# Kernel tuning notes

Measured on AMD Instinct MI355X. Metric: run time of the kernel, lower is better.

The kernel has to match this reference:

```python
import jax, jax.numpy as jnp
import numpy as np

N, E = 20000, 640000
D_IN, D_H, D_OUT = 128, 64, 32


def _lin_w(key, out_d, in_d):
    return jax.random.normal(key, (out_d, in_d), jnp.float32) / np.sqrt(in_d)


def setup_inputs() -> dict:
    key = jax.random.key(0)
    ks = jax.random.split(key, 16)
    x = jax.random.normal(ks[0], (N, D_IN), jnp.float32)
    edge_index = jax.random.randint(ks[1], (2, E), 0, N, jnp.int64)
    inp = {"x": x, "edge_index": edge_index}
    # SAGEConv weights: lin_l (aggregated neighbors, with bias), lin_r (root, no bias)
    inp["Wl1"] = _lin_w(ks[2], D_H, D_IN); inp["bl1"] = jnp.zeros((D_H,), jnp.float32)
    inp["Wr1"] = _lin_w(ks[3], D_H, D_IN)
    inp["Wl2"] = _lin_w(ks[4], D_H, D_H); inp["bl2"] = jnp.zeros((D_H,), jnp.float32)
    inp["Wr2"] = _lin_w(ks[5], D_H, D_H)
    inp["Wl3"] = _lin_w(ks[6], D_OUT, D_H); inp["bl3"] = jnp.zeros((D_OUT,), jnp.float32)
    inp["Wr3"] = _lin_w(ks[7], D_OUT, D_H)
    # Conv2d kernels (OIHW), all 3x3 pad 1
    inp["Wc1"] = jax.random.normal(ks[8], (D_H, 1, 3, 3), jnp.float32) / 3.0
    inp["bc1"] = jnp.zeros((D_H,), jnp.float32)
    inp["Wc2"] = jax.random.normal(ks[9], (D_H, D_H, 3, 3), jnp.float32) / np.sqrt(9 * D_H)
    inp["bc2"] = jnp.zeros((D_H,), jnp.float32)
    inp["Wc3"] = jax.random.normal(ks[10], (1, D_H, 3, 3), jnp.float32) / np.sqrt(9 * D_H)
    inp["bc3"] = jnp.zeros((1,), jnp.float32)
    # linear2 (hidden -> hidden)
    inp["W2"] = _lin_w(ks[11], D_H, D_H); inp["b2"] = jnp.zeros((D_H,), jnp.float32)
    return inp


def _sage(x, src, dst, Wl, bl, Wr):
    # PyG SAGEConv (mean aggr): lin_l(mean_{j->i} x_j) + lin_r(x_i)
    msg = x[src]  # [E, d] gather
    agg = jax.ops.segment_sum(msg, dst, num_segments=N)
    deg = jax.ops.segment_sum(jnp.ones((src.shape[0], 1), x.dtype), dst, num_segments=N)
    agg = agg / jnp.maximum(deg, 1.0)
    return agg @ Wl.T + bl + x @ Wr.T


def _conv(x, w, b):
    y = jax.lax.conv_general_dilated(x, w, (1, 1), ((1, 1), (1, 1)),
                                     dimension_numbers=("NCHW", "OIHW", "NCHW"))
    return y + b[None, :, None, None]


def reference(x, edge_index, Wl1, bl1, Wr1, Wl2, bl2, Wr2, Wl3, bl3, Wr3,
              Wc1, bc1, Wc2, bc2, Wc3, bc3, W2, b2):
    src, dst = edge_index[0], edge_index[1]
    h = _sage(x, src, dst, Wl1, bl1, Wr1)
    h = _sage(h, src, dst, Wl2, bl2, Wr2)
    h = _sage(h, src, dst, Wl2, bl2, Wr2)  # sage2 reused, as in source
    out_1 = h
    h4 = h[None, None]                     # [1,1,N,D_H]
    out = _conv(h4, Wc1, bc1)              # [1,D_H,N,D_H]
    out = _conv(out, Wc2, bc2)             # dropout is identity at inference
    out = _conv(out, Wc3, bc3)             # [1,1,N,D_H]
    out = out[0, 0] + out_1
    out = out @ W2.T + b2
    h = _sage(out, src, dst, Wl2, bl2, Wr2)
    h = _sage(h, src, dst, Wl2, bl2, Wr2)
    h = _sage(h, src, dst, Wl3, bl3, Wr3)
    return h
```

## Files before the change

kernel.cpp:

```cpp
#include <hip/hip_runtime.h>

#define NN 20000
#define NE 640000
#define NBUK 79

__device__ __forceinline__ int probe_stride(const int* __restrict__ ei32) {
  int lane = threadIdx.x & 63;
  int v = ei32[2 * lane + 1];
  unsigned long long nz = __ballot(v != 0);
  return (nz == 0ull) ? 2 : 1;
}

__device__ __forceinline__ bool maskB(int var, int o2, int o1) {
  int s = o2 + o1;
  switch (var) {
    case 0: return (o2 >= 0) && (s >= 0);
    case 1: return s >= -1;
    case 3: return s <= 1;
    case 4: return (o2 <= 0) && (s <= 0);
    default: return true;
  }
}

__global__ __launch_bounds__(256) void k_phaseA1(
    const int* __restrict__ ei, int* __restrict__ bhist,
    const float* __restrict__ Wc1, const float* __restrict__ Wc2,
    const float* __restrict__ Wc3, const float* __restrict__ bc1,
    const float* __restrict__ bc2, const float* __restrict__ bc3,
    const float* __restrict__ Wl1, const float* __restrict__ Wr1,
    const float* __restrict__ Wl2, const float* __restrict__ Wr2,
    const float* __restrict__ bl2,
    float* __restrict__ T729, float* __restrict__ beta5,
    float* __restrict__ Wt1, float* __restrict__ Wt2,
    float* __restrict__ Sbuf, float* __restrict__ c5,
    int* __restrict__ rowptr, int E, int N) {
  __shared__ float smem[6336];
  int b = blockIdx.x, tid = threadIdx.x;
  if (b >= 151) {
    int* lb = (int*)smem;
    int st = probe_stride(ei);
    for (int i = tid; i < NBUK; i += 256) lb[i] = 0;
    __syncthreads();
    int u = b - 151;
    int e0 = u * 4096;
#pragma unroll
    for (int t = 0; t < 16; ++t) {
      int e = e0 + t * 256 + tid;
      if (e < E) atomicAdd(&lb[ei[(size_t)(E + e) * st] >> 8], 1);
    }
    __syncthreads();
    for (int i = tid; i < NBUK; i += 256) bhist[u * NBUK + i] = lb[i];
    return;
  }
  int s = b;
  if (s == 0) {
    float* W3  = smem;
    float* S9s = smem + 576;
    float* W1s = smem + 5760;
    if (tid == 0) rowptr[N] = E;
    for (int e = tid; e < 576; e += 256) { W3[e] = Wc3[e]; W1s[e] = Wc1[e]; }
    __syncthreads();
    for (int bb = tid; bb < 576; bb += 256) {
      float acc[9];
#pragma unroll
      for (int a = 0; a < 9; ++a) acc[a] = 0.0f;
#pragma unroll 4
      for (int o = 0; o < 64; ++o) {
        float w2 = Wc2[o * 576 + bb];
#pragma unroll
        for (int a = 0; a < 9; ++a) acc[a] += W3[o * 9 + a] * w2;
      }
#pragma unroll
      for (int a = 0; a < 9; ++a) S9s[a * 576 + bb] = acc[a];
    }
    __syncthreads();
    for (int c = tid; c < 729; c += 256) {
      int kx0  = c % 3;
      int dl1e = (c / 3) % 3;
      int dl2e = (c / 9) % 3;
      int ky0  = (c / 27) % 3;
      int ky1  = (c / 81) % 3;
      int ky2  = c / 243;
      const float* s9 = &S9s[(ky2 * 3 + dl2e) * 576 + ky1 * 3 + dl1e];
      const float* w1 = &W1s[ky0 * 3 + kx0];
      float t = 0.0f;
#pragma unroll 8
      for (int i = 0; i < 64; ++i) t += s9[i * 9] * w1[i * 9];
      T729[c] = t;
    }
  } else if (s <= 5) {
    float* S2   = smem;
    float* W3b  = smem + 576;
    float* B2   = smem + 1152;
    float* part = smem + 1216;
    int var = s - 1;
    for (int e = tid; e < 576; e += 256) {
      int o = e / 9, r = e - o * 9;
      float t = 0.0f;
      for (int i = 0; i < 64; ++i) t += Wc2[o * 576 + i * 9 + r] * bc1[i];
      S2[e] = t;
      W3b[e] = Wc3[e];
    }
    if (tid < 64) B2[tid] = bc2[tid];
    __syncthreads();
    int u = tid & 63, oc = tid >> 6;
    float acc = 0.0f;
    for (int ky2 = 0; ky2 < 3; ++ky2) {
      int o2 = ky2 - 1;
      bool okA = (var == 0) ? (o2 >= 0) : (var == 4) ? (o2 <= 0) : true;
      if (!okA) continue;
      for (int dl2 = -1; dl2 <= 1; ++dl2) {
        int p = u + dl2; if ((unsigned)p >= 64u) continue;
        float sel[9];
#pragma unroll
        for (int ky1 = 0; ky1 < 3; ++ky1) {
          int o1 = ky1 - 1;
          bool mb = maskB(var, o2, o1);
#pragma unroll
          for (int dl1 = -1; dl1 <= 1; ++dl1) {
            int pq = p + dl1;
            sel[ky1 * 3 + dl1 + 1] = (mb && (unsigned)pq < 64u) ? 1.0f : 0.0f;
          }
        }
#pragma unroll 4
        for (int oo = 0; oo < 16; ++oo) {
          int o = oc * 16 + oo;
          float inner = B2[o];
#pragma unroll
          for (int r = 0; r < 9; ++r) inner += S2[o * 9 + r] * sel[r];
          acc += W3b[o * 9 + ky2 * 3 + (dl2 + 1)] * inner;
        }
      }
    }
    part[tid] = acc;
    __syncthreads();
    if (tid < 64) {
      beta5[var * 64 + tid] =
          bc3[0] + part[tid] + part[64 + tid] + part[128 + tid] + part[192 + tid];
    }
  } else {
    int idx = (s - 6) * 256 + tid;
    if (idx < 16384) {
      int w = idx >> 7, u = idx & 127;
      Wt1[idx] = (u < 64) ? Wl1[u * 128 + w] : Wr1[(u - 64) * 128 + w];
    } else if (idx < 24576) {
      int t = idx - 16384;
      int w = t >> 7, u = t & 127;
      Wt2[t] = (u < 64) ? Wl2[u * 64 + w] : Wr2[(u - 64) * 64 + w];
    } else if (idx < 36864) {
      int t2 = idx - 24576;
      int m = t2 >> 12, e = t2 & 4095;
      int i = e >> 6, j = e & 63;
      float acc = 0.0f;
#pragma unroll 4
      for (int k = 0; k < 64; ++k) {
        float wlj = Wl2[j * 64 + k], wrj = Wr2[j * 64 + k];
        float wli = Wl2[k * 64 + i], wri = Wr2[k * 64 + i];
        if (m == 0) acc += wli * wlj;
        else if (m == 1) acc += wri * wlj + wli * wrj;
        else acc += wri * wrj;
      }
      Sbuf[t2] = acc;
    } else if (idx < 36928) {
      int j = idx - 36864;
      float acc = bl2[j];
      for (int i = 0; i < 64; ++i)
        acc += bl2[i] * (Wl2[j * 64 + i] + Wr2[j * 64 + i]);
      c5[j] = acc;
    }
  }
}

__global__ __launch_bounds__(256) void k_phaseA2(
    const float* __restrict__ X, const float* __restrict__ Wt1,
    float* __restrict__ yzA,
    const int* __restrict__ ei, const int* __restrict__ bhist,
    unsigned long long* __restrict__ ebuf,
    const float* __restrict__ T729, float* __restrict__ M5T,
    const float* __restrict__ Sbuf, const float* __restrict__ c5,
    const float* __restrict__ Wl3, const float* __restrict__ Wr3,
    const float* __restrict__ bl3, float* __restrict__ Gbuf,
    float* __restrict__ c32, int E, int N) {
  __shared__ float smem[2048];
  int b = blockIdx.x, tid = threadIdx.x;
  if (b < 157) {
    int* lcnt  = (int*)smem;
    int* lbase = (int*)smem + 128;
    int* sscan = (int*)smem + 256;
    int st = probe_stride(ei);
    for (int i = tid; i < NBUK; i += 256) lcnt[i] = 0;
    int tot = 0, myoff = 0;
    if (tid < NBUK) {
      for (int v = 0; v < 157; ++v) {
        int h = bhist[v * NBUK + tid];
        tot += h;
        if (v < b) myoff += h;
      }
    }
    if (tid < 128) sscan[tid] = (tid < NBUK) ? tot : 0;
    __syncthreads();
    for (int off = 1; off < 128; off <<= 1) {
      int v = 0;
      if (tid < 128 && tid >= off) v = sscan[tid - off];
      __syncthreads();
      if (tid < 128) sscan[tid] += v;
      __syncthreads();
    }
    if (tid < NBUK) lbase[tid] = (sscan[tid] - tot) + myoff;
    __syncthreads();
    int e0 = b * 4096;
    int srcv[16], dstv[16], lrank[16], bk[16];
    int n = 0;
#pragma unroll
    for (int t = 0; t < 16; ++t) {
      int e = e0 + t * 256 + tid;
      if (e < E) {
        int sv = ei[(size_t)e * st];
        int d = ei[(size_t)(E + e) * st];
        int bb = d >> 8;
        srcv[n] = sv; dstv[n] = d; bk[n] = bb;
        lrank[n] = atomicAdd(&lcnt[bb], 1);
        ++n;
      }
    }
    for (int t = 0; t < n; ++t) {
      int pos = lbase[bk[t]] + lrank[t];
      ebuf[pos] = ((unsigned long long)(unsigned)dstv[t] << 32) | (unsigned)srcv[t];
    }
  } else if (b < 219) {
    float* Ts = smem;
    for (int e = tid; e < 729; e += 256) Ts[e] = T729[e];
    __syncthreads();
    int idx = (b - 157) * 256 + tid;
    if (idx >= 15680) return;
    int jw = idx % 7;
    int u  = (idx / 7) % 64;
    int d  = (idx / 448) % 7;
    int var = idx / 3136;
    int w = u + jw - 3;
    float acc = 0.0f;
    if (w >= 0 && w < 64) {
      for (int ky2 = 0; ky2 < 3; ++ky2) {
        int o2 = ky2 - 1;
        for (int ky1 = 0; ky1 < 3; ++ky1) {
          int o1 = ky1 - 1;
          if (!maskB(var, o2, o1)) continue;
          int o0 = (d - 3) - o2 - o1;
          if (o0 < -1 || o0 > 1) continue;
          int ky0 = o0 + 1;
          int cbase = ((ky2 * 3 + ky1) * 3 + ky0) * 27;
#pragma unroll
          for (int kx0 = 0; kx0 < 3; ++kx0) {
            int jq = jw - kx0;
            if ((unsigned)jq >= 5u) continue;
            int q = u + jq - 2;
            if ((unsigned)q >= 64u) continue;
#pragma unroll
            for (int dl2e = 0; dl2e < 3; ++dl2e) {
              int p = u + dl2e - 1;
              if ((unsigned)p >= 64u) continue;
              int dl1e = jq - dl2e;
              if ((unsigned)dl1e >= 3u) continue;
              acc += Ts[cbase + dl2e * 9 + dl1e * 3 + kx0];
            }
          }
        }
      }
    }
    if (d == 3 && jw == 3) acc += 1.0f;
    M5T[(var * 49 + d * 7 + jw) * 64 + u] = acc;
  } else if (b < 252) {
    int bb = b - 219;
    if (bb < 32) {
      int idx = bb * 256 + tid;
      int kblk = idx >> 11;
      int rem = idx & 2047;
      int t = rem >> 5, j = rem & 31;
      const float* S2p = Sbuf;
      const float* S1p = Sbuf + 4096;
      const float* S0p = Sbuf + 8192;
      const float* pa = (kblk == 0) ? S2p : (kblk == 1) ? S1p : (kblk == 2) ? S0p : nullptr;
      const float* pb = (kblk == 1) ? S2p : (kblk == 2) ? S1p : (kblk == 3) ? S0p : nullptr;
      float acc = 0.0f;
#pragma unroll 4
      for (int k = 0; k < 64; ++k) {
        if (pa) acc += pa[t * 64 + k] * Wl3[j * 64 + k];
        if (pb) acc += pb[t * 64 + k] * Wr3[j * 64 + k];
      }
      Gbuf[idx] = acc;
    } else if (tid < 32) {
      float acc = bl3[tid];
      for (int k = 0; k < 64; ++k)
        acc += c5[k] * (Wl3[tid * 64 + k] + Wr3[tid * 64 + k]);
      c32[tid] = acc;
    }
  } else {
    constexpr int C = 128, K = 128, ROWS = 16, RPT = ROWS * C / 256;
    float* Xs = smem;
    int y0 = (b - 252) * ROWS;
    {
      const float4* src = (const float4*)(X + (size_t)y0 * K);
      float4* dst = (float4*)Xs;
#pragma unroll
      for (int v = 0; v < ROWS * K / 4 / 256; ++v)
        dst[v * 256 + tid] = src[v * 256 + tid];
    }
    __syncthreads();
    int u = tid % C;
    int rg = tid / C;
    float acc[RPT];
#pragma unroll
    for (int k = 0; k < RPT; ++k) acc[k] = 0.0f;
#pragma unroll 2
    for (int w0 = 0; w0 < K; w0 += 4) {
      float m0 = Wt1[(w0 + 0) * C + u];
      float m1 = Wt1[(w0 + 1) * C + u];
      float m2 = Wt1[(w0 + 2) * C + u];
      float m3 = Wt1[(w0 + 3) * C + u];
      const float* xs = &Xs[(rg * RPT) * K + w0];
#pragma unroll
      for (int k = 0; k < RPT; ++k) {
        float4 h = *(const float4*)(xs + k * K);
        acc[k] += m0 * h.x + m1 * h.y + m2 * h.z + m3 * h.w;
      }
    }
#pragma unroll
    for (int k = 0; k < RPT; ++k)
      yzA[(size_t)(y0 + rg * RPT + k) * C + u] = acc[k];
  }
}

__global__ __launch_bounds__(256) void k_phaseA3(
    const unsigned long long* __restrict__ ebuf, const int* __restrict__ bhist,
    int* __restrict__ rowptr, float* __restrict__ invdeg,
    int* __restrict__ csr,
    const float* __restrict__ Gbuf, const float* __restrict__ W2,
    const float* __restrict__ b2, float* __restrict__ Wg,
    float* __restrict__ bg, int N) {
  __shared__ int smem[772];
  int b = blockIdx.x, tid = threadIdx.x;
  if (b < NBUK) {
    int* lcnt  = smem;
    int* lcur  = smem + 256;
    int* wsum  = smem + 512;
    int* sscan = smem + 516;
    int* tots  = smem + 644;
    int tot = 0;
    if (tid < NBUK)
      for (int v = 0; v < 157; ++v) tot += bhist[v * NBUK + tid];
    if (tid < 128) { tots[tid] = (tid < NBUK) ? tot : 0; sscan[tid] = tots ? ((tid < NBUK) ? tot : 0) : 0; }
    __syncthreads();
    for (int off = 1; off < 128; off <<= 1) {
      int v = 0;
      if (tid < 128 && tid >= off) v = sscan[tid - off];
      __syncthreads();
      if (tid < 128) sscan[tid] += v;
      __syncthreads();
    }
    if (tid < 128) sscan[tid] -= tots[tid];
    __syncthreads();
    int base = sscan[b];
    int n = tots[b];
    lcnt[tid] = 0;
    __syncthreads();
    for (int e = tid; e < n; e += 256) {
      int d = (int)(ebuf[base + e] >> 32);
      atomicAdd(&lcnt[d - (b << 8)], 1);
    }
    __syncthreads();
    int c = lcnt[tid];
    int lane = tid & 63, wid = tid >> 6;
    int s = c;
#pragma unroll
    for (int off = 1; off < 64; off <<= 1) {
      int v = __shfl_up(s, off, 64);
      if (lane >= off) s += v;
    }
    if (lane == 63) wsum[wid] = s;
    __syncthreads();
    int woff = 0;
    for (int w = 0; w < wid; ++w) woff += wsum[w];
    int pref = woff + s - c;
    int gnode = (b << 8) + tid;
    if (gnode < N) {
      rowptr[gnode] = base + pref;
      invdeg[gnode] = 1.0f / (float)(c < 1 ? 1 : c);
    }
    lcur[tid] = pref;
    __syncthreads();
    for (int e = tid; e < n; e += 256) {
      unsigned long long pk = ebuf[base + e];
      int d = (int)(pk >> 32);
      int pos = atomicAdd(&lcur[d - (b << 8)], 1);
      csr[base + pos] = (int)(unsigned)pk;
    }
  } else {
    int bb = b - NBUK;
    if (bb < 32) {
      int idx = bb * 256 + tid;
      int w = idx >> 7, u = idx & 127;
      int kblk = u >> 5, j = u & 31;
      const float* gp = Gbuf + kblk * 2048 + j;
      float acc = 0.0f;
#pragma unroll 4
      for (int t = 0; t < 64; ++t) acc += W2[t * 64 + w] * gp[t * 32];
      Wg[idx] = acc;
    } else if (tid < 128) {
      int kblk = tid >> 5, j = tid & 31;
      const float* gp = Gbuf + kblk * 2048 + j;
      float acc = 0.0f;
      for (int t = 0; t < 64; ++t) acc += b2[t] * gp[t * 32];
      bg[tid] = acc;
    }
  }
}

template <int C>
__global__ __launch_bounds__(256) void k_fused(const float* __restrict__ yzin,
                                               const int* __restrict__ csr,
                                               const int* __restrict__ rowptr,
                                               const float* __restrict__ invdeg,
                                               const float* __restrict__ bl,
                                               const float* __restrict__ Wt,
                                               float* __restrict__ out, int N) {
  constexpr int FV = 16;
  constexpr int G  = 4;
  constexpr int S4 = 32;
  constexpr int CAP = 64;
  __shared__ int idxs[16 * CAP];
  __shared__ float htile[16 * 64];
  int tid = threadIdx.x;
  int w = tid >> 6, lane = tid & 63;
  int base = blockIdx.x * 16;
  int beg_r[4], m_r[4], end_r[4];
#pragma unroll
  for (int rr = 0; rr < 4; ++rr) {
    int node = base + w * 4 + rr;
    int beg = rowptr[node], end = rowptr[node + 1];
    beg_r[rr] = beg; end_r[rr] = end;
    int cnt = end - beg;
    int m = cnt < CAP ? cnt : CAP;
    m_r[rr] = m;
    int* my = &idxs[(w * 4 + rr) * CAP];
    for (int k = lane; k < m; k += 64) my[k] = csr[beg + k];
  }
  __syncthreads();
  int g = lane / FV, f = lane % FV;
  const float4* yz4 = (const float4*)yzin;
#pragma unroll
  for (int rr = 0; rr < 4; ++rr) {
    int node = base + w * 4 + rr;
    const int* my = &idxs[(w * 4 + rr) * CAP];
    int m = m_r[rr];
    float a0x=0,a0y=0,a0z=0,a0w=0, a1x=0,a1y=0,a1z=0,a1w=0;
    float a2x=0,a2y=0,a2z=0,a2w=0, a3x=0,a3y=0,a3z=0,a3w=0;
    int j = g;
    for (; j + 3 * G < m; j += 4 * G) {
      int s0 = my[j], s1 = my[j + G], s2 = my[j + 2 * G], s3 = my[j + 3 * G];
      float4 v0 = yz4[(size_t)s0 * S4 + f];
      float4 v1 = yz4[(size_t)s1 * S4 + f];
      float4 v2 = yz4[(size_t)s2 * S4 + f];
      float4 v3 = yz4[(size_t)s3 * S4 + f];
      a0x += v0.x; a0y += v0.y; a0z += v0.z; a0w += v0.w;
      a1x += v1.x; a1y += v1.y; a1z += v1.z; a1w += v1.w;
      a2x += v2.x; a2y += v2.y; a2z += v2.z; a2w += v2.w;
      a3x += v3.x; a3y += v3.y; a3z += v3.z; a3w += v3.w;
    }
    for (; j < m; j += G) {
      int s0 = my[j];
      float4 v0 = yz4[(size_t)s0 * S4 + f];
      a0x += v0.x; a0y += v0.y; a0z += v0.z; a0w += v0.w;
    }
    for (int jj = beg_r[rr] + CAP + g; jj < end_r[rr]; jj += G) {
      int s0 = csr[jj];
      float4 v0 = yz4[(size_t)s0 * S4 + f];
      a0x += v0.x; a0y += v0.y; a0z += v0.z; a0w += v0.w;
    }
    float ax = (a0x + a1x) + (a2x + a3x);
    float ay = (a0y + a1y) + (a2y + a3y);
    float az = (a0z + a1z) + (a2z + a3z);
    float aw = (a0w + a1w) + (a2w + a3w);
#pragma unroll
    for (int mm = FV; mm < 64; mm <<= 1) {
      ax += __shfl_xor(ax, mm, 64);
      ay += __shfl_xor(ay, mm, 64);
      az += __shfl_xor(az, mm, 64);
      aw += __shfl_xor(aw, mm, 64);
    }
    if (g == 0) {
      float4 root = yz4[(size_t)node * S4 + FV + f];
      float4 bv = ((const float4*)bl)[f];
      float id = invdeg[node];
      float4 o;
      o.x = ax * id + bv.x + root.x;
      o.y = ay * id + bv.y + root.y;
      o.z = az * id + bv.z + root.z;
      o.w = aw * id + bv.w + root.w;
      ((float4*)htile)[(w * 4 + rr) * 16 + f] = o;
    }
  }
  __syncthreads();
  constexpr int RPT = 16 * C / 256;
  int u = tid % C, rg = tid / C;
  float acc[RPT];
#pragma unroll
  for (int k = 0; k < RPT; ++k) acc[k] = 0.0f;
#pragma unroll 2
  for (int w0 = 0; w0 < 64; w0 += 4) {
    float m0 = Wt[(w0 + 0) * C + u];
    float m1 = Wt[(w0 + 1) * C + u];
    float m2 = Wt[(w0 + 2) * C + u];
    float m3 = Wt[(w0 + 3) * C + u];
    const float* xs = &htile[(rg * RPT) * 64 + w0];
#pragma unroll
    for (int k = 0; k < RPT; ++k) {
      float4 h4 = *(const float4*)(xs + k * 64);
      acc[k] += m0 * h4.x + m1 * h4.y + m2 * h4.z + m3 * h4.w;
    }
  }
#pragma unroll
  for (int k = 0; k < RPT; ++k)
    out[(size_t)(base + rg * RPT + k) * C + u] = acc[k];
}

__global__ __launch_bounds__(256) void k_applyfused(
    const float* __restrict__ h, const float* __restrict__ M5T,
    const float* __restrict__ beta5, const float* __restrict__ Wg,
    const float* __restrict__ bg, float* __restrict__ wout, int N) {
  __shared__ float hs[22 * 70];
  __shared__ float htile[16 * 64];
  int tid = threadIdx.x;
  int bstart = blockIdx.x * 16;
  for (int idx = tid; idx < 22 * 70; idx += 256) {
    int row = idx / 70, col = idx - row * 70;
    int y = bstart - 3 + row;
    int ww = col - 3;
    float v = 0.0f;
    if ((unsigned)y < (unsigned)N && (unsigned)ww < 64u)
      v = h[(size_t)y * 64 + ww];
    hs[idx] = v;
  }
  __syncthreads();
  int u = tid & 63, g = tid >> 6;
  int lr0 = g * 4;
  int gstart = bstart + lr0;
  const float* basep = &hs[lr0 * 70 + u];
  bool interior = (gstart >= 2) && (gstart + 3 <= N - 3);
  if (interior) {
    float c[49];
#pragma unroll
    for (int t = 0; t < 49; ++t) c[t] = M5T[(2 * 49 + t) * 64 + u];
    float bet = beta5[2 * 64 + u];
    float acc[4];
#pragma unroll
    for (int k = 0; k < 4; ++k) acc[k] = bet;
#pragma unroll
    for (int rr = 0; rr < 10; ++rr) {
      float t7[7];
#pragma unroll
      for (int jw = 0; jw < 7; ++jw) t7[jw] = basep[rr * 70 + jw];
#pragma unroll
      for (int d = 0; d < 7; ++d) {
        int k = rr - d;
        if (k >= 0 && k < 4) {
#pragma unroll
          for (int jw = 0; jw < 7; ++jw) acc[k] += c[d * 7 + jw] * t7[jw];
        }
      }
    }
#pragma unroll
    for (int k = 0; k < 4; ++k) htile[(lr0 + k) * 64 + u] = acc[k];
  } else {
    for (int k = 0; k < 4; ++k) {
      int y = gstart + k;
      int var = (y == 0) ? 0 : (y == 1) ? 1 : (y == N - 2) ? 3 : (y == N - 1) ? 4 : 2;
      float acc = beta5[var * 64 + u];
      for (int d = 0; d < 7; ++d)
        for (int jw = 0; jw < 7; ++jw)
          acc += M5T[(var * 49 + d * 7 + jw) * 64 + u] * basep[(k + d) * 70 + jw];
      htile[(lr0 + k) * 64 + u] = acc;
    }
  }
  __syncthreads();
  int u2 = tid % 128, rg = tid / 128;
  float acc2[8];
  float bv = bg[u2];
#pragma unroll
  for (int k = 0; k < 8; ++k) acc2[k] = bv;
#pragma unroll 2
  for (int w0 = 0; w0 < 64; w0 += 4) {
    float m0 = Wg[(w0 + 0) * 128 + u2];
    float m1 = Wg[(w0 + 1) * 128 + u2];
    float m2 = Wg[(w0 + 2) * 128 + u2];
    float m3 = Wg[(w0 + 3) * 128 + u2];
    const float* xs = &htile[(rg * 8) * 64 + w0];
#pragma unroll
    for (int k = 0; k < 8; ++k) {
      float4 h4 = *(const float4*)(xs + k * 64);
      acc2[k] += m0 * h4.x + m1 * h4.y + m2 * h4.z + m3 * h4.w;
    }
  }
  int kb = u2 >> 5, jj = u2 & 31;
#pragma unroll
  for (int k = 0; k < 8; ++k) {
    int node = bstart + rg * 8 + k;
    wout[((size_t)kb * N + node) * 32 + jj] = acc2[k];
  }
}

template <int DH>
__global__ __launch_bounds__(256) void k_agg(const float* __restrict__ yz,
                                             const int* __restrict__ csr,
                                             const int* __restrict__ rowptr,
                                             const float* __restrict__ invdeg,
                                             const float* __restrict__ bl,
                                             float* __restrict__ out, int N) {
  constexpr int FV = DH / 4;
  constexpr int G  = 64 / FV;
  constexpr int S4 = DH / 2;
  constexpr int CAP = 256;
  __shared__ int idxs[4 * CAP];
  int wid = threadIdx.x >> 6, lane = threadIdx.x & 63;
  int node = blockIdx.x * 4 + wid;
  int beg = rowptr[node], end = rowptr[node + 1];
  int cnt = end - beg;
  int m = cnt < CAP ? cnt : CAP;
  int* my = &idxs[wid * CAP];
  for (int k = lane; k < m; k += 64) my[k] = csr[beg + k];
  __syncthreads();
  int g = lane / FV, f = lane % FV;
  const float4* yz4 = (const float4*)yz;
  float a0x=0,a0y=0,a0z=0,a0w=0, a1x=0,a1y=0,a1z=0,a1w=0;
  float a2x=0,a2y=0,a2z=0,a2w=0, a3x=0,a3y=0,a3z=0,a3w=0;
  int j = g;
  for (; j + 3 * G < m; j += 4 * G) {
    int s0 = my[j], s1 = my[j + G], s2 = my[j + 2 * G], s3 = my[j + 3 * G];
    float4 v0 = yz4[(size_t)s0 * S4 + f];
    float4 v1 = yz4[(size_t)s1 * S4 + f];
    float4 v2 = yz4[(size_t)s2 * S4 + f];
    float4 v3 = yz4[(size_t)s3 * S4 + f];
    a0x += v0.x; a0y += v0.y; a0z += v0.z; a0w += v0.w;
    a1x += v1.x; a1y += v1.y; a1z += v1.z; a1w += v1.w;
    a2x += v2.x; a2y += v2.y; a2z += v2.z; a2w += v2.w;
    a3x += v3.x; a3y += v3.y; a3z += v3.z; a3w += v3.w;
  }
  for (; j < m; j += G) {
    int s0 = my[j];
    float4 v0 = yz4[(size_t)s0 * S4 + f];
    a0x += v0.x; a0y += v0.y; a0z += v0.z; a0w += v0.w;
  }
  for (int jj = beg + CAP + g; jj < end; jj += G) {
    int s0 = csr[jj];
    float4 v0 = yz4[(size_t)s0 * S4 + f];
    a0x += v0.x; a0y += v0.y; a0z += v0.z; a0w += v0.w;
  }
  float ax = (a0x + a1x) + (a2x + a3x);
  float ay = (a0y + a1y) + (a2y + a3y);
  float az = (a0z + a1z) + (a2z + a3z);
  float aw = (a0w + a1w) + (a2w + a3w);
#pragma unroll
  for (int mm = FV; mm < 64; mm <<= 1) {
    ax += __shfl_xor(ax, mm, 64);
    ay += __shfl_xor(ay, mm, 64);
    az += __shfl_xor(az, mm, 64);
    aw += __shfl_xor(aw, mm, 64);
  }
  if (g == 0) {
    float4 root = yz4[(size_t)node * S4 + FV + f];
    float4 bv = ((const float4*)bl)[f];
    float id = invdeg[node];
    float4 o;
    o.x = ax * id + bv.x + root.x;
    o.y = ay * id + bv.y + root.y;
    o.z = az * id + bv.z + root.z;
    o.w = aw * id + bv.w + root.w;
    ((float4*)out)[(size_t)node * FV + f] = o;
  }
}

__global__ __launch_bounds__(256) void k_agg32(
    const float* __restrict__ src, const int* __restrict__ csr,
    const int* __restrict__ rowptr, const float* __restrict__ invdeg,
    const float* __restrict__ add, const float* __restrict__ cvec,
    float* __restrict__ out, int N) {
  constexpr int FV = 8;
  constexpr int G  = 8;
  constexpr int CAP = 256;
  __shared__ int idxs[4 * CAP];
  int wid = threadIdx.x >> 6, lane = threadIdx.x & 63;
  int node = blockIdx.x * 4 + wid;
  int beg = rowptr[node], end = rowptr[node + 1];
  int cnt = end - beg;
  int m = cnt < CAP ? cnt : CAP;
  int* my = &idxs[wid * CAP];
  for (int k = lane; k < m; k += 64) my[k] = csr[beg + k];
  __syncthreads();
  int g = lane / FV, f = lane % FV;
  const float4* sr4 = (const float4*)src;
  float a0x=0,a0y=0,a0z=0,a0w=0, a1x=0,a1y=0,a1z=0,a1w=0;
  float a2x=0,a2y=0,a2z=0,a2w=0, a3x=0,a3y=0,a3z=0,a3w=0;
  int j = g;
  for (; j + 3 * G < m; j += 4 * G) {
    int s0 = my[j], s1 = my[j + G], s2 = my[j + 2 * G], s3 = my[j + 3 * G];
    float4 v0 = sr4[(size_t)s0 * FV + f];
    float4 v1 = sr4[(size_t)s1 * FV + f];
    float4 v2 = sr4[(size_t)s2 * FV + f];
    float4 v3 = sr4[(size_t)s3 * FV + f];
    a0x += v0.x; a0y += v0.y; a0z += v0.z; a0w += v0.w;
    a1x += v1.x; a1y += v1.y; a1z += v1.z; a1w += v1.w;
    a2x += v2.x; a2y += v2.y; a2z += v2.z; a2w += v2.w;
    a3x += v3.x; a3y += v3.y; a3z += v3.z; a3w += v3.w;
  }
  for (; j < m; j += G) {
    int s0 = my[j];
    float4 v0 = sr4[(size_t)s0 * FV + f];
    a0x += v0.x; a0y += v0.y; a0z += v0.z; a0w += v0.w;
  }
  for (int jj = beg + CAP + g; jj < end; jj += G) {
    int s0 = csr[jj];
    float4 v0 = sr4[(size_t)s0 * FV + f];
    a0x += v0.x; a0y += v0.y; a0z += v0.z; a0w += v0.w;
  }
  float ax = (a0x + a1x) + (a2x + a3x);
  float ay = (a0y + a1y) + (a2y + a3y);
  float az = (a0z + a1z) + (a2z + a3z);
  float aw = (a0w + a1w) + (a2w + a3w);
#pragma unroll
  for (int mm = FV; mm < 64; mm <<= 1) {
    ax += __shfl_xor(ax, mm, 64);
    ay += __shfl_xor(ay, mm, 64);
    az += __shfl_xor(az, mm, 64);
    aw += __shfl_xor(aw, mm, 64);
  }
  if (g == 0) {
    float4 av = ((const float4*)add)[(size_t)node * FV + f];
    float id = invdeg[node];
    float4 o;
    o.x = ax * id + av.x;
    o.y = ay * id + av.y;
    o.z = az * id + av.z;
    o.w = aw * id + av.w;
    if (cvec != nullptr) {
      float4 cv = ((const float4*)cvec)[f];
      o.x += cv.x; o.y += cv.y; o.z += cv.z; o.w += cv.w;
    }
    ((float4*)out)[(size_t)node * FV + f] = o;
  }
}

extern "C" void kernel_launch(void* const* d_in, const int* in_sizes, int n_in,
                              void* d_out, int out_size, void* d_ws, size_t ws_size,
                              hipStream_t stream) {
  const int N = NN, E = NE;
  const float* x   = (const float*)d_in[0];
  const int*   ei  = (const int*)d_in[1];
  const float* Wl1 = (const float*)d_in[2];
  const float* bl1 = (const float*)d_in[3];
  const float* Wr1 = (const float*)d_in[4];
  const float* Wl2 = (const float*)d_in[5];
  const float* bl2 = (const float*)d_in[6];
  const float* Wr2 = (const float*)d_in[7];
  const float* Wl3 = (const float*)d_in[8];
  const float* bl3 = (const float*)d_in[9];
  const float* Wr3 = (const float*)d_in[10];
  const float* Wc1 = (const float*)d_in[11];
  const float* bc1 = (const float*)d_in[12];
  const float* Wc2 = (const float*)d_in[13];
  const float* bc2 = (const float*)d_in[14];
  const float* Wc3 = (const float*)d_in[15];
  const float* bc3 = (const float*)d_in[16];
  const float* W2  = (const float*)d_in[17];
  const float* b2  = (const float*)d_in[18];

  char* ws = (char*)d_ws;
  size_t off = 0;
  auto alloc = [&](size_t bytes) -> void* {
    off = (off + 255) & ~(size_t)255;
    void* p = ws + off;
    off += bytes;
    return p;
  };
  int*   rowptr  = (int*)alloc((size_t)(N + 1) * 4);
  float* invdeg  = (float*)alloc((size_t)N * 4);
  int*   csr     = (int*)alloc((size_t)E * 4);
  unsigned long long* ebuf = (unsigned long long*)alloc((size_t)E * 8);
  int*   bhist   = (int*)alloc(157 * NBUK * 4);
  float* Wt1     = (float*)alloc(128 * 128 * 4);
  float* Wt2     = (float*)alloc(64 * 128 * 4);
  float* T729    = (float*)alloc(729 * 4);
  float* M5T     = (float*)alloc(15680 * 4);
  float* beta5   = (float*)alloc(320 * 4);
  float* Sbuf    = (float*)alloc(12288 * 4);
  float* c5      = (float*)alloc(64 * 4);
  float* Gbuf    = (float*)alloc(8192 * 4);
  float* Wg      = (float*)alloc(8192 * 4);
  float* bg      = (float*)alloc(128 * 4);
  float* c32     = (float*)alloc(32 * 4);
  float* yzA     = (float*)alloc((size_t)N * 128 * 4);
  float* yzB     = (float*)alloc((size_t)N * 128 * 4);
  float* hA      = (float*)alloc((size_t)N * 64 * 4);
  float* wbuf    = (float*)alloc((size_t)4 * N * 32 * 4);
  float* s1buf   = (float*)alloc((size_t)N * 32 * 4);
  float* s2buf   = (float*)alloc((size_t)N * 32 * 4);
  (void)ws_size; (void)in_sizes; (void)n_in; (void)out_size;

  const int gG = N / 16;
  const int gA = N / 4;

  k_phaseA1<<<308, 256, 0, stream>>>(ei, bhist, Wc1, Wc2, Wc3, bc1, bc2, bc3,
                                     Wl1, Wr1, Wl2, Wr2, bl2,
                                     T729, beta5, Wt1, Wt2, Sbuf, c5,
                                     rowptr, E, N);
  k_phaseA2<<<1502, 256, 0, stream>>>(x, Wt1, yzA, ei, bhist, ebuf,
                                      T729, M5T, Sbuf, c5, Wl3, Wr3, bl3,
                                      Gbuf, c32, E, N);
  k_phaseA3<<<112, 256, 0, stream>>>(ebuf, bhist, rowptr, invdeg, csr,
                                     Gbuf, W2, b2, Wg, bg, N);

  k_fused<128><<<gG, 256, 0, stream>>>(yzA, csr, rowptr, invdeg, bl1, Wt2, yzB, N);
  k_fused<128><<<gG, 256, 0, stream>>>(yzB, csr, rowptr, invdeg, bl2, Wt2, yzA, N);
  k_agg<64><<<gA, 256, 0, stream>>>(yzA, csr, rowptr, invdeg, bl2, hA, N);
  k_applyfused<<<gG, 256, 0, stream>>>(hA, M5T, beta5, Wg, bg, wbuf, N);
  const float* w3  = wbuf;
  const float* w2p = wbuf + (size_t)N * 32;
  const float* w1p = wbuf + (size_t)2 * N * 32;
  const float* w0p = wbuf + (size_t)3 * N * 32;
  k_agg32<<<gA, 256, 0, stream>>>(w3, csr, rowptr, invdeg, w2p, nullptr, s1buf, N);
  k_agg32<<<gA, 256, 0, stream>>>(s1buf, csr, rowptr, invdeg, w1p, nullptr, s2buf, N);
  k_agg32<<<gA, 256, 0, stream>>>(s2buf, csr, rowptr, invdeg, w0p, c32, (float*)d_out, N);
}
```

Measured before the change: 278.6 us.

## Store gathered neighbor features in bf16 to halve gather traffic

Splits the combined yz buffers into a bf16 half (the part gathered over edges) and an fp32 half (the root term), and stores the propagated 32-wide intermediates as bf16. All aggregation kernels are rewritten to load packed bf16 as uint4 and accumulate in fp32 with new lane mappings. This targets the memory bandwidth of the random edge gathers, which dominate the runtime. The cost is reduced precision in the aggregated features, which is repeated across six layers.

```diff
diff --git a/kernel.cpp b/kernel.cpp
--- a/kernel.cpp
+++ b/kernel.cpp
@@ -3,6 +3,33 @@
 #define NN 20000
 #define NE 640000
 #define NBUK 79
+
+__device__ __forceinline__ unsigned short f2b(float f) {
+  unsigned int u = __float_as_uint(f);
+  u += 0x7FFFu + ((u >> 16) & 1u);
+  return (unsigned short)(u >> 16);
+}
+__device__ __forceinline__ float blo(unsigned int w) {
+  return __uint_as_float(w << 16);
+}
+__device__ __forceinline__ float bhi(unsigned int w) {
+  return __uint_as_float(w & 0xFFFF0000u);
+}
+__device__ __forceinline__ void bacc8(float* a, uint4 v) {
+  a[0] += blo(v.x); a[1] += bhi(v.x);
+  a[2] += blo(v.y); a[3] += bhi(v.y);
+  a[4] += blo(v.z); a[5] += bhi(v.z);
+  a[6] += blo(v.w); a[7] += bhi(v.w);
+}
+__device__ __forceinline__ void bget8(float* a, uint4 v) {
+  a[0] = blo(v.x); a[1] = bhi(v.x);
+  a[2] = blo(v.y); a[3] = bhi(v.y);
+  a[4] = blo(v.z); a[5] = bhi(v.z);
+  a[6] = blo(v.w); a[7] = bhi(v.w);
+}
+__device__ __forceinline__ unsigned int pk2(float lo, float hi) {
+  return (unsigned int)f2b(lo) | ((unsigned int)f2b(hi) << 16);
+}
 
 __device__ __forceinline__ int probe_stride(const int* __restrict__ ei32) {
   int lane = threadIdx.x & 63;
@@ -173,7 +200,7 @@
 
 __global__ __launch_bounds__(256) void k_phaseA2(
     const float* __restrict__ X, const float* __restrict__ Wt1,
-    float* __restrict__ yzA,
+    unsigned short* __restrict__ ybA, float* __restrict__ zfA,
     const int* __restrict__ ei, const int* __restrict__ bhist,
     unsigned long long* __restrict__ ebuf,
     const float* __restrict__ T729, float* __restrict__ M5T,
@@ -324,9 +351,16 @@
         acc[k] += m0 * h.x + m1 * h.y + m2 * h.z + m3 * h.w;
       }
     }
-#pragma unroll
-    for (int k = 0; k < RPT; ++k)
-      yzA[(size_t)(y0 + rg * RPT + k) * C + u] = acc[k];
+    if (u < 64) {
+#pragma unroll
+      for (int k = 0; k < RPT; ++k)
+        ybA[(size_t)(y0 + rg * RPT + k) * 64 + u] = f2b(acc[k]);
+    } else {
+      int uz = u - 64;
+#pragma unroll
+      for (int k = 0; k < RPT; ++k)
+        zfA[(size_t)(y0 + rg * RPT + k) * 64 + uz] = acc[k];
+    }
   }
 }
 
@@ -348,7 +382,11 @@
     int tot = 0;
     if (tid < NBUK)
       for (int v = 0; v < 157; ++v) tot += bhist[v * NBUK + tid];
-    if (tid < 128) { tots[tid] = (tid < NBUK) ? tot : 0; sscan[tid] = tots ? ((tid < NBUK) ? tot : 0) : 0; }
+    if (tid < 128) {
+      int tv = (tid < NBUK) ? tot : 0;
+      tots[tid] = tv;
+      sscan[tid] = tv;
+    }
     __syncthreads();
     for (int off = 1; off < 128; off <<= 1) {
       int v = 0;
@@ -415,17 +453,12 @@
   }
 }
 
-template <int C>
-__global__ __launch_bounds__(256) void k_fused(const float* __restrict__ yzin,
-                                               const int* __restrict__ csr,
-                                               const int* __restrict__ rowptr,
-                                               const float* __restrict__ invdeg,
-                                               const float* __restrict__ bl,
-                                               const float* __restrict__ Wt,
-                                               float* __restrict__ out, int N) {
-  constexpr int FV = 16;
-  constexpr int G  = 4;
-  constexpr int S4 = 32;
+__global__ __launch_bounds__(256) void k_fusedb(
+    const unsigned short* __restrict__ yb, const float* __restrict__ zf,
+    const int* __restrict__ csr, const int* __restrict__ rowptr,
+    const float* __restrict__ invdeg, const float* __restrict__ bl,
+    const float* __restrict__ Wt, unsigned short* __restrict__ ybo,
+    float* __restrict__ zfo, int N) {
   constexpr int CAP = 64;
   __shared__ int idxs[16 * CAP];
   __shared__ float htile[16 * 64];
@@ -445,88 +478,124 @@
     for (int k = lane; k < m; k += 64) my[k] = csr[beg + k];
   }
   __syncthreads();
-  int g = lane / FV, f = lane % FV;
-  const float4* yz4 = (const float4*)yzin;
+  int g = lane >> 3, f = lane & 7;
+  const uint4* yb4 = (const uint4*)yb;
 #pragma unroll
   for (int rr = 0; rr < 4; ++rr) {
     int node = base + w * 4 + rr;
     const int* my = &idxs[(w * 4 + rr) * CAP];
     int m = m_r[rr];
-    float a0x=0,a0y=0,a0z=0,a0w=0, a1x=0,a1y=0,a1z=0,a1w=0;
-    float a2x=0,a2y=0,a2z=0,a2w=0, a3x=0,a3y=0,a3z=0,a3w=0;
+    float a[8] = {0, 0, 0, 0, 0, 0, 0, 0};
+    float bacc[8] = {0, 0, 0, 0, 0, 0, 0, 0};
     int j = g;
-    for (; j + 3 * G < m; j += 4 * G) {
-      int s0 = my[j], s1 = my[j + G], s2 = my[j + 2 * G], s3 = my[j + 3 * G];
-      float4 v0 = yz4[(size_t)s0 * S4 + f];
-      float4 v1 = yz4[(size_t)s1 * S4 + f];
-      float4 v2 = yz4[(size_t)s2 * S4 + f];
-      float4 v3 = yz4[(size_t)s3 * S4 + f];
-      a0x += v0.x; a0y += v0.y; a0z += v0.z; a0w += v0.w;
-      a1x += v1.x; a1y += v1.y; a1z += v1.z; a1w += v1.w;
-      a2x += v2.x; a2y += v2.y; a2z += v2.z; a2w += v2.w;
-      a3x += v3.x; a3y += v3.y; a3z += v3.z; a3w += v3.w;
-    }
-    for (; j < m; j += G) {
-      int s0 = my[j];
-      float4 v0 = yz4[(size_t)s0 * S4 + f];
-      a0x += v0.x; a0y += v0.y; a0z += v0.z; a0w += v0.w;
-    }
-    for (int jj = beg_r[rr] + CAP + g; jj < end_r[rr]; jj += G) {
-      int s0 = csr[jj];
-      float4 v0 = yz4[(size_t)s0 * S4 + f];
-      a0x += v0.x; a0y += v0.y; a0z += v0.z; a0w += v0.w;
-    }
-    float ax = (a0x + a1x) + (a2x + a3x);
-    float ay = (a0y + a1y) + (a2y + a3y);
-    float az = (a0z + a1z) + (a2z + a3z);
-    float aw = (a0w + a1w) + (a2w + a3w);
-#pragma unroll
-    for (int mm = FV; mm < 64; mm <<= 1) {
-      ax += __shfl_xor(ax, mm, 64);
-      ay += __shfl_xor(ay, mm, 64);
-      az += __shfl_xor(az, mm, 64);
-      aw += __shfl_xor(aw, mm, 64);
-    }
+    for (; j + 8 < m; j += 16) {
+      int s0 = my[j], s1 = my[j + 8];
+      uint4 v0 = yb4[(size_t)s0 * 8 + f];
+      uint4 v1 = yb4[(size_t)s1 * 8 + f];
+      bacc8(a, v0);
+      bacc8(bacc, v1);
+    }
+    for (; j < m; j += 8) bacc8(a, yb4[(size_t)my[j] * 8 + f]);
+    for (int jj = beg_r[rr] + CAP + g; jj < end_r[rr]; jj += 8)
+      bacc8(a, yb4[(size_t)csr[jj] * 8 + f]);
+#pragma unroll
+    for (int i = 0; i < 8; ++i) a[i] += bacc[i];
+#pragma unroll
+    for (int mm = 8; mm < 64; mm <<= 1)
+#pragma unroll
+      for (int i = 0; i < 8; ++i) a[i] += __shfl_xor(a[i], mm, 64);
     if (g == 0) {
-      float4 root = yz4[(size_t)node * S4 + FV + f];
-      float4 bv = ((const float4*)bl)[f];
       float id = invdeg[node];
-      float4 o;
-      o.x = ax * id + bv.x + root.x;
-      o.y = ay * id + bv.y + root.y;
-      o.z = az * id + bv.z + root.z;
-      o.w = aw * id + bv.w + root.w;
-      ((float4*)htile)[(w * 4 + rr) * 16 + f] = o;
+      const float* zr = zf + (size_t)node * 64 + f * 8;
+      const float* bp = bl + f * 8;
+      float* ht = &htile[(w * 4 + rr) * 64 + f * 8];
+#pragma unroll
+      for (int i = 0; i < 8; ++i) ht[i] = a[i] * id + bp[i] + zr[i];
     }
   }
   __syncthreads();
-  constexpr int RPT = 16 * C / 256;
-  int u = tid % C, rg = tid / C;
-  float acc[RPT];
-#pragma unroll
-  for (int k = 0; k < RPT; ++k) acc[k] = 0.0f;
+  int u = tid & 127, rg = tid >> 7;
+  float acc[8];
+#pragma unroll
+  for (int k = 0; k < 8; ++k) acc[k] = 0.0f;
 #pragma unroll 2
   for (int w0 = 0; w0 < 64; w0 += 4) {
-    float m0 = Wt[(w0 + 0) * C + u];
-    float m1 = Wt[(w0 + 1) * C + u];
-    float m2 = Wt[(w0 + 2) * C + u];
-    float m3 = Wt[(w0 + 3) * C + u];
-    const float* xs = &htile[(rg * RPT) * 64 + w0];
-#pragma unroll
-    for (int k = 0; k < RPT; ++k) {
+    float m0 = Wt[(w0 + 0) * 128 + u];
+    float m1 = Wt[(w0 + 1) * 128 + u];
+    float m2 = Wt[(w0 + 2) * 128 + u];
+    float m3 = Wt[(w0 + 3) * 128 + u];
+    const float* xs = &htile[(rg * 8) * 64 + w0];
+#pragma unroll
+    for (int k = 0; k < 8; ++k) {
       float4 h4 = *(const float4*)(xs + k * 64);
       acc[k] += m0 * h4.x + m1 * h4.y + m2 * h4.z + m3 * h4.w;
     }
   }
-#pragma unroll
-  for (int k = 0; k < RPT; ++k)
-    out[(size_t)(base + rg * RPT + k) * C + u] = acc[k];
-}
-
-__global__ __launch_bounds__(256) void k_applyfused(
+  if (u < 64) {
+#pragma unroll
+    for (int k = 0; k < 8; ++k)
+      ybo[(size_t)(base + rg * 8 + k) * 64 + u] = f2b(acc[k]);
+  } else {
+    int uz = u - 64;
+#pragma unroll
+    for (int k = 0; k < 8; ++k)
+      zfo[(size_t)(base + rg * 8 + k) * 64 + uz] = acc[k];
+  }
+}
+
+__global__ __launch_bounds__(256) void k_aggb64(
+    const unsigned short* __restrict__ yb, const float* __restrict__ zf,
+    const int* __restrict__ csr, const int* __restrict__ rowptr,
+    const float* __restrict__ invdeg, const float* __restrict__ bl,
+    float* __restrict__ out, int N) {
+  constexpr int CAP = 256;
+  __shared__ int idxs[4 * CAP];
+  int wid = threadIdx.x >> 6, lane = threadIdx.x & 63;
+  int node = blockIdx.x * 4 + wid;
+  int beg = rowptr[node], end = rowptr[node + 1];
+  int cnt = end - beg;
+  int m = cnt < CAP ? cnt : CAP;
+  int* my = &idxs[wid * CAP];
+  for (int k = lane; k < m; k += 64) my[k] = csr[beg + k];
+  __syncthreads();
+  int g = lane >> 3, f = lane & 7;
+  const uint4* yb4 = (const uint4*)yb;
+  float a[8] = {0, 0, 0, 0, 0, 0, 0, 0};
+  float bacc[8] = {0, 0, 0, 0, 0, 0, 0, 0};
+  int j = g;
+  for (; j + 8 < m; j += 16) {
+    int s0 = my[j], s1 = my[j + 8];
+    uint4 v0 = yb4[(size_t)s0 * 8 + f];
+    uint4 v1 = yb4[(size_t)s1 * 8 + f];
+    bacc8(a, v0);
+    bacc8(bacc, v1);
+  }
+  for (; j < m; j += 8) bacc8(a, yb4[(size_t)my[j] * 8 + f]);
+  for (int jj = beg + CAP + g; jj < end; jj += 8)
+    bacc8(a, yb4[(size_t)csr[jj] * 8 + f]);
+#pragma unroll
+  for (int i = 0; i < 8; ++i) a[i] += bacc[i];
+#pragma unroll
+  for (int mm = 8; mm < 64; mm <<= 1)
+#pragma unroll
+    for (int i = 0; i < 8; ++i) a[i] += __shfl_xor(a[i], mm, 64);
+  if (g == 0) {
+    float id = invdeg[node];
+    const float* zr = zf + (size_t)node * 64 + f * 8;
+    const float* bp = bl + f * 8;
+    float o[8];
+#pragma unroll
+    for (int i = 0; i < 8; ++i) o[i] = a[i] * id + bp[i] + zr[i];
+    float* op = out + (size_t)node * 64 + f * 8;
+    ((float4*)op)[0] = make_float4(o[0], o[1], o[2], o[3]);
+    ((float4*)op)[1] = make_float4(o[4], o[5], o[6], o[7]);
+  }
+}
+
+__global__ __launch_bounds__(256) void k_applyb(
     const float* __restrict__ h, const float* __restrict__ M5T,
     const float* __restrict__ beta5, const float* __restrict__ Wg,
-    const float* __restrict__ bg, float* __restrict__ wout, int N) {
+    const float* __restrict__ bg, unsigned short* __restrict__ wout, int N) {
   __shared__ float hs[22 * 70];
   __shared__ float htile[16 * 64];
   int tid = threadIdx.x;
@@ -604,20 +673,15 @@
 #pragma unroll
   for (int k = 0; k < 8; ++k) {
     int node = bstart + rg * 8 + k;
-    wout[((size_t)kb * N + node) * 32 + jj] = acc2[k];
-  }
-}
-
-template <int DH>
-__global__ __launch_bounds__(256) void k_agg(const float* __restrict__ yz,
-                                             const int* __restrict__ csr,
-                                             const int* __restrict__ rowptr,
-                                             const float* __restrict__ invdeg,
-                                             const float* __restrict__ bl,
-                                             float* __restrict__ out, int N) {
-  constexpr int FV = DH / 4;
-  constexpr int G  = 64 / FV;
-  constexpr int S4 = DH / 2;
+    wout[((size_t)kb * N + node) * 32 + jj] = f2b(acc2[k]);
+  }
+}
+
+__global__ __launch_bounds__(256) void k_agg32b(
+    const unsigned short* __restrict__ src, const int* __restrict__ csr,
+    const int* __restrict__ rowptr, const float* __restrict__ invdeg,
+    const unsigned short* __restrict__ addb, const float* __restrict__ cvec,
+    unsigned short* __restrict__ outb, float* __restrict__ outf, int N) {
   constexpr int CAP = 256;
   __shared__ int idxs[4 * CAP];
   int wid = threadIdx.x >> 6, lane = threadIdx.x & 63;
@@ -628,123 +692,48 @@
   int* my = &idxs[wid * CAP];
   for (int k = lane; k < m; k += 64) my[k] = csr[beg + k];
   __syncthreads();
-  int g = lane / FV, f = lane % FV;
-  const float4* yz4 = (const float4*)yz;
-  float a0x=0,a0y=0,a0z=0,a0w=0, a1x=0,a1y=0,a1z=0,a1w=0;
-  float a2x=0,a2y=0,a2z=0,a2w=0, a3x=0,a3y=0,a3z=0,a3w=0;
+  int g = lane >> 2, f = lane & 3;
+  const uint4* sr4 = (const uint4*)src;
+  float a[8] = {0, 0, 0, 0, 0, 0, 0, 0};
+  float bacc[8] = {0, 0, 0, 0, 0, 0, 0, 0};
   int j = g;
-  for (; j + 3 * G < m; j += 4 * G) {
-    int s0 = my[j], s1 = my[j + G], s2 = my[j + 2 * G], s3 = my[j + 3 * G];
-    float4 v0 = yz4[(size_t)s0 * S4 + f];
-    float4 v1 = yz4[(size_t)s1 * S4 + f];
-    float4 v2 = yz4[(size_t)s2 * S4 + f];
-    float4 v3 = yz4[(size_t)s3 * S4 + f];
-    a0x += v0.x; a0y += v0.y; a0z += v0.z; a0w += v0.w;
-    a1x += v1.x; a1y += v1.y; a1z += v1.z; a1w += v1.w;
-    a2x += v2.x; a2y += v2.y; a2z += v2.z; a2w += v2.w;
-    a3x += v3.x; a3y += v3.y; a3z += v3.z; a3w += v3.w;
-  }
-  for (; j < m; j += G) {
-    int s0 = my[j];
-    float4 v0 = yz4[(size_t)s0 * S4 + f];
-    a0x += v0.x; a0y += v0.y; a0z += v0.z; a0w += v0.w;
-  }
-  for (int jj = beg + CAP + g; jj < end; jj += G) {
-    int s0 = csr[jj];
-    float4 v0 = yz4[(size_t)s0 * S4 + f];
-    a0x += v0.x; a0y += v0.y; a0z += v0.z; a0w += v0.w;
-  }
-  float ax = (a0x + a1x) + (a2x + a3x);
-  float ay = (a0y + a1y) + (a2y + a3y);
-  float az = (a0z + a1z) + (a2z + a3z);
-  float aw = (a0w + a1w) + (a2w + a3w);
-#pragma unroll
-  for (int mm = FV; mm < 64; mm <<= 1) {
-    ax += __shfl_xor(ax, mm, 64);
-    ay += __shfl_xor(ay, mm, 64);
-    az += __shfl_xor(az, mm, 64);
-    aw += __shfl_xor(aw, mm, 64);
-  }
+  for (; j + 16 < m; j += 32) {
+    int s0 = my[j], s1 = my[j + 16];
+    uint4 v0 = sr4[(size_t)s0 * 4 + f];
+    uint4 v1 = sr4[(size_t)s1 * 4 + f];
+    bacc8(a, v0);
+    bacc8(bacc, v1);
+  }
+  for (; j < m; j += 16) bacc8(a, sr4[(size_t)my[j] * 4 + f]);
+  for (int jj = beg + CAP + g; jj < end; jj += 16)
+    bacc8(a, sr4[(size_t)csr[jj] * 4 + f]);
+#pragma unroll
+  for (int i = 0; i < 8; ++i) a[i] += bacc[i];
+#pragma unroll
+  for (int mm = 4; mm < 64; mm <<= 1)
+#pragma unroll
+    for (int i = 0; i < 8; ++i) a[i] += __shfl_xor(a[i], mm, 64);
   if (g == 0) {
-    float4 root = yz4[(size_t)node * S4 + FV + f];
-    float4 bv = ((const float4*)bl)[f];
     float id = invdeg[node];
-    float4 o;
-    o.x = ax * id + bv.x + root.x;
-    o.y = ay * id + bv.y + root.y;
-    o.z = az * id + bv.z + root.z;
-    o.w = aw * id + bv.w + root.w;
-    ((float4*)out)[(size_t)node * FV + f] = o;
-  }
-}
-
-__global__ __launch_bounds__(256) void k_agg32(
-    const float* __restrict__ src, const int* __restrict__ csr,
-    const int* __restrict__ rowptr, const float* __restrict__ invdeg,
-    const float* __restrict__ add, const float* __restrict__ cvec,
-    float* __restrict__ out, int N) {
-  constexpr int FV = 8;
-  constexpr int G  = 8;
-  constexpr int CAP = 256;
-  __shared__ int idxs[4 * CAP];
-  int wid = threadIdx.x >> 6, lane = threadIdx.x & 63;
-  int node = blockIdx.x * 4 + wid;
-  int beg = rowptr[node], end = rowptr[node + 1];
-  int cnt = end - beg;
-  int m = cnt < CAP ? cnt : CAP;
-  int* my = &idxs[wid * CAP];
-  for (int k = lane; k < m; k += 64) my[k] = csr[beg + k];
-  __syncthreads();
-  int g = lane / FV, f = lane % FV;
-  const float4* sr4 = (const float4*)src;
-  float a0x=0,a0y=0,a0z=0,a0w=0, a1x=0,a1y=0,a1z=0,a1w=0;
-  float a2x=0,a2y=0,a2z=0,a2w=0, a3x=0,a3y=0,a3z=0,a3w=0;
-  int j = g;
-  for (; j + 3 * G < m; j += 4 * G) {
-    int s0 = my[j], s1 = my[j + G], s2 = my[j + 2 * G], s3 = my[j + 3 * G];
-    float4 v0 = sr4[(size_t)s0 * FV + f];
-    float4 v1 = sr4[(size_t)s1 * FV + f];
-    float4 v2 = sr4[(size_t)s2 * FV + f];
-    float4 v3 = sr4[(size_t)s3 * FV + f];
-    a0x += v0.x; a0y += v0.y; a0z += v0.z; a0w += v0.w;
-    a1x += v1.x; a1y += v1.y; a1z += v1.z; a1w += v1.w;
-    a2x += v2.x; a2y += v2.y; a2z += v2.z; a2w += v2.w;
-    a3x += v3.x; a3y += v3.y; a3z += v3.z; a3w += v3.w;
-  }
-  for (; j < m; j += G) {
-    int s0 = my[j];
-    float4 v0 = sr4[(size_t)s0 * FV + f];
-    a0x += v0.x; a0y += v0.y; a0z += v0.z; a0w += v0.w;
-  }
-  for (int jj = beg + CAP + g; jj < end; jj += G) {
-    int s0 = csr[jj];
-    float4 v0 = sr4[(size_t)s0 * FV + f];
-    a0x += v0.x; a0y += v0.y; a0z += v0.z; a0w += v0.w;
-  }
-  float ax = (a0x + a1x) + (a2x + a3x);
-  float ay = (a0y + a1y) + (a2y + a3y);
-  float az = (a0z + a1z) + (a2z + a3z);
-  float aw = (a0w + a1w) + (a2w + a3w);
-#pragma unroll
-  for (int mm = FV; mm < 64; mm <<= 1) {
-    ax += __shfl_xor(ax, mm, 64);
-    ay += __shfl_xor(ay, mm, 64);
-    az += __shfl_xor(az, mm, 64);
-    aw += __shfl_xor(aw, mm, 64);
-  }
-  if (g == 0) {
-    float4 av = ((const float4*)add)[(size_t)node * FV + f];
-    float id = invdeg[node];
-    float4 o;
-    o.x = ax * id + av.x;
-    o.y = ay * id + av.y;
-    o.z = az * id + av.z;
-    o.w = aw * id + av.w;
+    float ad[8];
+    bget8(ad, ((const uint4*)addb)[(size_t)node * 4 + f]);
+    float o[8];
+#pragma unroll
+    for (int i = 0; i < 8; ++i) o[i] = a[i] * id + ad[i];
     if (cvec != nullptr) {
-      float4 cv = ((const float4*)cvec)[f];
-      o.x += cv.x; o.y += cv.y; o.z += cv.z; o.w += cv.w;
-    }
-    ((float4*)out)[(size_t)node * FV + f] = o;
+#pragma unroll
+      for (int i = 0; i < 8; ++i) o[i] += cvec[f * 8 + i];
+    }
+    if (outb != nullptr) {
+      uint4 pv;
+      pv.x = pk2(o[0], o[1]); pv.y = pk2(o[2], o[3]);
+      pv.z = pk2(o[4], o[5]); pv.w = pk2(o[6], o[7]);
+      ((uint4*)outb)[(size_t)node * 4 + f] = pv;
+    } else {
+      float* op = outf + (size_t)node * 32 + f * 8;
+      ((float4*)op)[0] = make_float4(o[0], o[1], o[2], o[3]);
+      ((float4*)op)[1] = make_float4(o[4], o[5], o[6], o[7]);
+    }
   }
 }
 
@@ -796,12 +785,14 @@
   float* Wg      = (float*)alloc(8192 * 4);
   float* bg      = (float*)alloc(128 * 4);
   float* c32     = (float*)alloc(32 * 4);
-  float* yzA     = (float*)alloc((size_t)N * 128 * 4);
-  float* yzB     = (float*)alloc((size_t)N * 128 * 4);
+  unsigned short* ybA = (unsigned short*)alloc((size_t)N * 64 * 2);
+  unsigned short* ybB = (unsigned short*)alloc((size_t)N * 64 * 2);
+  float* zfA     = (float*)alloc((size_t)N * 64 * 4);
+  float* zfB     = (float*)alloc((size_t)N * 64 * 4);
   float* hA      = (float*)alloc((size_t)N * 64 * 4);
-  float* wbuf    = (float*)alloc((size_t)4 * N * 32 * 4);
-  float* s1buf   = (float*)alloc((size_t)N * 32 * 4);
-  float* s2buf   = (float*)alloc((size_t)N * 32 * 4);
+  unsigned short* wb  = (unsigned short*)alloc((size_t)4 * N * 32 * 2);
+  unsigned short* s1b = (unsigned short*)alloc((size_t)N * 32 * 2);
+  unsigned short* s2b = (unsigned short*)alloc((size_t)N * 32 * 2);
   (void)ws_size; (void)in_sizes; (void)n_in; (void)out_size;
 
   const int gG = N / 16;
@@ -811,21 +802,26 @@
                                      Wl1, Wr1, Wl2, Wr2, bl2,
                                      T729, beta5, Wt1, Wt2, Sbuf, c5,
                                      rowptr, E, N);
-  k_phaseA2<<<1502, 256, 0, stream>>>(x, Wt1, yzA, ei, bhist, ebuf,
+  k_phaseA2<<<1502, 256, 0, stream>>>(x, Wt1, ybA, zfA, ei, bhist, ebuf,
                                       T729, M5T, Sbuf, c5, Wl3, Wr3, bl3,
                                       Gbuf, c32, E, N);
   k_phaseA3<<<112, 256, 0, stream>>>(ebuf, bhist, rowptr, invdeg, csr,
                                      Gbuf, W2, b2, Wg, bg, N);
 
-  k_fused<128><<<gG, 256, 0, stream>>>(yzA, csr, rowptr, invdeg, bl1, Wt2, yzB, N);
-  k_fused<128><<<gG, 256, 0, stream>>>(yzB, csr, rowptr, invdeg, bl2, Wt2, yzA, N);
-  k_agg<64><<<gA, 256, 0, stream>>>(yzA, csr, rowptr, invdeg, bl2, hA, N);
-  k_applyfused<<<gG, 256, 0, stream>>>(hA, M5T, beta5, Wg, bg, wbuf, N);
-  const float* w3  = wbuf;
-  const float* w2p = wbuf + (size_t)N * 32;
-  const float* w1p = wbuf + (size_t)2 * N * 32;
-  const float* w0p = wbuf + (size_t)3 * N * 32;
-  k_agg32<<<gA, 256, 0, stream>>>(w3, csr, rowptr, invdeg, w2p, nullptr, s1buf, N);
-  k_agg32<<<gA, 256, 0, stream>>>(s1buf, csr, rowptr, invdeg, w1p, nullptr, s2buf, N);
-  k_agg32<<<gA, 256, 0, stream>>>(s2buf, csr, rowptr, invdeg, w0p, c32, (float*)d_out, N);
-}
+  k_fusedb<<<gG, 256, 0, stream>>>(ybA, zfA, csr, rowptr, invdeg, bl1, Wt2,
+                                   ybB, zfB, N);
+  k_fusedb<<<gG, 256, 0, stream>>>(ybB, zfB, csr, rowptr, invdeg, bl2, Wt2,
+                                   ybA, zfA, N);
+  k_aggb64<<<gA, 256, 0, stream>>>(ybA, zfA, csr, rowptr, invdeg, bl2, hA, N);
+  k_applyb<<<gG, 256, 0, stream>>>(hA, M5T, beta5, Wg, bg, wb, N);
+  const unsigned short* w3  = wb;
+  const unsigned short* w2p = wb + (size_t)N * 32;
+  const unsigned short* w1p = wb + (size_t)2 * N * 32;
+  const unsigned short* w0p = wb + (size_t)3 * N * 32;
+  k_agg32b<<<gA, 256, 0, stream>>>(w3, csr, rowptr, invdeg, w2p, nullptr,
+                                   s1b, nullptr, N);
+  k_agg32b<<<gA, 256, 0, stream>>>(s1b, csr, rowptr, invdeg, w1p, nullptr,
+                                   s2b, nullptr, N);
+  k_agg32b<<<gA, 256, 0, stream>>>(s2b, csr, rowptr, invdeg, w0p, c32,
+                                   nullptr, (float*)d_out, N);
+}
```

Result: no change. 279.8 us (+0.4%).
